# Kernel tuning notes

Measured on AMD Instinct MI355X. Metric: run time of the kernel, lower is better.

## Reference

```python
import jax, jax.numpy as jnp
import numpy as np

N = 50000   # nodes
E = 600000  # edges (time_feat is per-edge: same mask indexes k and src_idx)
D = 128     # adapter_dim
C = 8       # num_clusters
SCALE = D ** -0.5


def setup_inputs() -> dict:
    key = jax.random.key(0)
    ks = jax.random.split(key, 12)
    s = 1.0 / np.sqrt(D)
    return {
        "node_feat": jax.random.normal(ks[0], (N, D), jnp.float32),
        "time_feat": jax.random.normal(ks[1], (E, D), jnp.float32),
        "context_feat": jax.random.normal(ks[2], (N, D), jnp.float32),
        "edge_index": jax.random.randint(ks[3], (2, E), 0, N),
        "Wq": jax.random.uniform(ks[4], (D, D), jnp.float32, -s, s),
        "bq": jnp.zeros((D,), jnp.float32),
        "Wk": jax.random.uniform(ks[5], (D, D), jnp.float32, -s, s),
        "bk": jnp.zeros((D,), jnp.float32),
        "Wv": jax.random.uniform(ks[6], (D, D), jnp.float32, -s, s),
        "bv": jnp.zeros((D,), jnp.float32),
        "cluster_emb": jax.random.normal(ks[7], (C, D), jnp.float32),
        "Wo": jax.random.uniform(ks[8], (D, D), jnp.float32, -s, s),
        "bo": jnp.zeros((D,), jnp.float32),
    }


def reference(node_feat, time_feat, context_feat, edge_index,
              Wq, bq, Wk, bk, Wv, bv, cluster_emb, Wo, bo):
    q = node_feat @ Wq + bq            # [N, D]
    k = time_feat @ Wk + bk            # [E, D]
    v = time_feat @ Wv + bv            # [E, D]

    # cluster routing: argmax(softmax(sim)) == argmax(sim)
    sim = (time_feat @ cluster_emb.T) * SCALE   # [E, C]
    assign = jnp.argmax(sim, axis=-1)           # [E] int

    src = edge_index[0]                          # [E]
    seg = assign * N + src                       # combined (cluster, dst-of-scatter) segment id
    nseg = C * N

    attn = jnp.sum(q[src] * k, axis=-1) * SCALE  # [E]

    # scatter_softmax per (cluster, src node)
    seg_max = jax.ops.segment_max(attn, seg, num_segments=nseg)
    ex = jnp.exp(attn - seg_max[seg])
    denom = jax.ops.segment_sum(ex, seg, num_segments=nseg)
    w = ex / denom[seg]                          # [E]

    # scatter_mean per (cluster, src node) -> [C, N, D]
    wv = v * w[:, None]
    sums = jax.ops.segment_sum(wv, seg, num_segments=nseg)                 # [C*N, D]
    counts = jax.ops.segment_sum(jnp.ones((E,), v.dtype), seg, num_segments=nseg)
    means = sums / jnp.maximum(counts, 1.0)[:, None]                       # empty -> 0
    per_cluster = means.reshape(C, N, D)

    # sum(outputs) / len(outputs): only non-empty clusters contribute an entry
    edges_per_cluster = jax.ops.segment_sum(jnp.ones((E,), jnp.float32), assign, num_segments=C)
    num_nonempty = jnp.sum((edges_per_cluster > 0).astype(jnp.float32))
    combined = per_cluster.sum(axis=0) / num_nonempty                      # [N, D]

    return jax.nn.relu(combined @ Wo + bo)
```

## Files before the change

kernel.cpp:

```cpp
#include <hip/hip_runtime.h>
#include <math.h>


#define NN 50000
#define NE 600000
#define DD 128
#define NC 8
#define WIN 64
#define NWIN 9376
#define NBF  9377
#define CHK 32
#define NLOC 64
#define SCALEF 0.08838834764831845f

#define OFF_NODECNT  0
#define OFF_FILL     50000
#define OFF_MASK     100000
#define ZERO_ELEMS   100256
#define OFF_NODEOFF  100352
#define OFF_PARTIAL  150352
#define OFF_BF       150608
#define OFF_BQK      160000
#define OFF_BVO      160128
#define OFF_WQBK     160256
#define OFF_C0       160384
#define OFF_WQK      160400
#define OFF_WVO      176784
#define OFF_QB       193168
#define OFF_SORTED   243168
#define OFF_SRCS     843168
#define OFF_SW       1443168
#define OFF_P        1493168

__global__ __launch_bounds__(256) void k_pre_count(
    const float* __restrict__ Wq, const float* __restrict__ bq,
    const float* __restrict__ Wk, const float* __restrict__ bk,
    const float* __restrict__ Wv, const float* __restrict__ bv,
    const float* __restrict__ Wo, const int* __restrict__ ei,
    int* __restrict__ node_cnt,
    float* __restrict__ Wqk, float* __restrict__ bqk,
    float* __restrict__ Wvo, float* __restrict__ bvo,
    float* __restrict__ wqbk, float* __restrict__ c0) {
  int bid = blockIdx.x, t = threadIdx.x;
  if (bid >= 129) {
    long e = (long)(bid - 129) * 256 + t;
    if (e < NE) atomicAdd(&node_cnt[ei[e]], 1);
    return;
  }
  __shared__ float rq[DD], rv[DD];
  int b = bid;
  if (b < DD) {
    if (t < DD) { rq[t] = Wq[b * DD + t]; rv[t] = Wv[b * DD + t]; }
    __syncthreads();
    if (t < DD) {
      float aq = 0.f, av = 0.f;
      for (int j = 0; j < DD; j++) {
        aq += rq[j] * Wk[t * DD + j];
        av += rv[j] * Wo[j * DD + t];
      }
      Wqk[b * DD + t] = aq;
      Wvo[b * DD + t] = av;
    }
  } else {
    if (t < DD) {
      float a1 = 0.f, a2 = 0.f, a3 = 0.f;
      for (int j = 0; j < DD; j++) {
        a1 += bq[j] * Wk[t * DD + j];
        a2 += bv[j] * Wo[j * DD + t];
        a3 += Wq[t * DD + j] * bk[j];
      }
      bqk[t] = a1; bvo[t] = a2; wqbk[t] = a3;
      if (t == 0) {
        float s = 0.f;
        for (int j = 0; j < DD; j++) s += bq[j] * bk[j];
        *c0 = s;
      }
    }
  }
}

__global__ __launch_bounds__(256) void k_p(
    const float* __restrict__ nf, const float* __restrict__ Wqk,
    const float* __restrict__ bqk, const float* __restrict__ wqbk,
    const float* __restrict__ c0p,
    float* __restrict__ p, float* __restrict__ qb) {
  __shared__ float a_lds[64 * DD];
  __shared__ float wb_lds[DD];
  int t = threadIdx.x;
  long row0 = (long)blockIdx.x * 64;
  for (int it = 0; it < 8; it++) {
    int idx = (it * 256 + t) * 4;
    long r = row0 + idx / DD;
    float4 v = {0.f, 0.f, 0.f, 0.f};
    if (r < NN) v = *(const float4*)(nf + r * DD + (idx % DD));
    *(float4*)(a_lds + idx) = v;
  }
  if (t < DD) wb_lds[t] = wqbk[t];
  __syncthreads();
  int cg = t % 32, rg = t / 32;
  int col0 = cg * 4, r0 = rg * 8;
  float acc[8][4]; float qacc[8];
  for (int r = 0; r < 8; r++) { qacc[r] = 0.f; for (int c = 0; c < 4; c++) acc[r][c] = 0.f; }
  for (int k = 0; k < DD; k++) {
    float4 b4 = *(const float4*)(Wqk + k * DD + col0);
    float wbk = wb_lds[k];
    for (int r = 0; r < 8; r++) {
      float a = a_lds[(r0 + r) * DD + k];
      acc[r][0] += a * b4.x; acc[r][1] += a * b4.y;
      acc[r][2] += a * b4.z; acc[r][3] += a * b4.w;
      qacc[r] += a * wbk;
    }
  }
  float4 bq4 = *(const float4*)(bqk + col0);
  float c0v = *c0p;
  for (int r = 0; r < 8; r++) {
    long row = row0 + r0 + r;
    if (row < NN) {
      float4 o;
      o.x = acc[r][0] + bq4.x; o.y = acc[r][1] + bq4.y;
      o.z = acc[r][2] + bq4.z; o.w = acc[r][3] + bq4.w;
      *(float4*)(p + row * DD + col0) = o;
      if (cg == 0) qb[row] = qacc[r] + c0v;
    }
  }
}

__global__ __launch_bounds__(256) void k_scan1(const int* __restrict__ node_cnt,
                                               int* __restrict__ partial) {
  int i = blockIdx.x * 256 + threadIdx.x;
  int v = (i < NN) ? node_cnt[i] : 0;
  for (int o = 1; o < 64; o <<= 1) v += __shfl_xor(v, o);
  __shared__ int wsum[4];
  if ((threadIdx.x & 63) == 0) wsum[threadIdx.x >> 6] = v;
  __syncthreads();
  if (threadIdx.x == 0) partial[blockIdx.x] = wsum[0] + wsum[1] + wsum[2] + wsum[3];
}

__global__ __launch_bounds__(256) void k_scan2(int* __restrict__ partial) {
  __shared__ int s[256];
  int t = threadIdx.x;
  int v = (t < 196) ? partial[t] : 0;
  s[t] = v;
  __syncthreads();
  for (int o = 1; o < 256; o <<= 1) {
    int add = (t >= o) ? s[t - o] : 0;
    __syncthreads();
    s[t] += add;
    __syncthreads();
  }
  if (t < 196) partial[t] = s[t] - v;
}

__global__ __launch_bounds__(256) void k_scan3(const int* __restrict__ node_cnt,
                                               const int* __restrict__ partial,
                                               int* __restrict__ node_off) {
  __shared__ int s[256];
  int t = threadIdx.x;
  int i = blockIdx.x * 256 + t;
  int v = (i < NN) ? node_cnt[i] : 0;
  s[t] = v;
  __syncthreads();
  for (int o = 1; o < 256; o <<= 1) {
    int add = (t >= o) ? s[t - o] : 0;
    __syncthreads();
    s[t] += add;
    __syncthreads();
  }
  if (i < NN) node_off[i] = partial[blockIdx.x] + s[t] - v;
}

#define EDGE_BLKS 2344
#define BS_BLKS   37
__global__ __launch_bounds__(256) void k_scatter(const int* __restrict__ ei,
                                                 const int* __restrict__ node_off,
                                                 int* __restrict__ fill,
                                                 int* __restrict__ sorted,
                                                 int* __restrict__ srcs,
                                                 int* __restrict__ blockFirst) {
  int bid = blockIdx.x, t = threadIdx.x;
  if (bid >= EDGE_BLKS) {
    int w = (bid - EDGE_BLKS) * 256 + t;
    if (w < NBF) {
      int v = w * WIN, lo = 0, hi = NN;
      while (lo < hi) { int mid = (lo + hi) >> 1; if (node_off[mid] < v) lo = mid + 1; else hi = mid; }
      blockFirst[w] = lo;
    }
    return;
  }
  long e = (long)bid * 256 + t;
  if (e < NE) {
    int s = ei[e];
    int pos = node_off[s] + atomicAdd(&fill[s], 1);
    sorted[pos] = (int)e;
    srcs[pos] = s;
  }
}

__global__ __launch_bounds__(256) void k_fused2(
    const float* __restrict__ tf, const int* __restrict__ sorted,
    const int* __restrict__ srcs, const int* __restrict__ node_off,
    const int* __restrict__ node_cnt, const int* __restrict__ blockFirst,
    const float* __restrict__ ce, const float* __restrict__ p,
    const float* __restrict__ qb, int* __restrict__ maskArr,
    float* __restrict__ agg, float* __restrict__ sw) {
  __shared__ float ce_lds[NC * DD];
  __shared__ float t_lds[CHK * DD];
  __shared__ float U_sh[NC * DD];
  __shared__ float D_sh[NLOC * NC];
  __shared__ int   C_sh[NLOC * NC];
  __shared__ float exf_sh[CHK];
  __shared__ int   cli_sh[CHK];
  __shared__ int   eidx_sh[CHK];
  __shared__ int   srcs_sh[CHK];
  __shared__ int   cnt0_sh[NLOC];

  int t = threadIdx.x, b = blockIdx.x;
  int fn = blockFirst[b], ln = blockFirst[b + 1] - 1;
  if (fn >= NN || ln < fn) return;

  *(float4*)(ce_lds + t * 4) = *(const float4*)(ce + t * 4);

  int el = t >> 3, j = t & 7;
  int d = t & 127;
  int msk_acc = 0;

  for (int s0 = fn; s0 <= ln; s0 += NLOC) {
    int e2 = s0 + NLOC - 1; if (e2 > ln) e2 = ln;
    int nN = e2 - s0 + 1;
    int eb = node_off[s0];
    int ee = node_off[e2] + node_cnt[e2];
    for (int i = t; i < NLOC * NC; i += 256) { D_sh[i] = 0.f; C_sh[i] = 0; }
    for (int i = t; i < NC * DD; i += 256) U_sh[i] = 0.f;
    if (t < nN) cnt0_sh[t] = node_cnt[s0 + t];
    __syncthreads();

    for (int n = 0; n < nN; n++) {
      if (cnt0_sh[n] == 0) {
        if (t < DD) agg[(long)(s0 + n) * DD + t] = 0.f;
        if (t == 0) sw[s0 + n] = 0.f;
      }
    }

    int cur = -1;
    auto do_flush = [&](int node) {
      int l = (node - s0) * NC;
      if (t < DD) {
        float acc = 0.f;
        #pragma unroll
        for (int c = 0; c < NC; c++) {
          int cc = C_sh[l + c];
          if (cc > 0)
            acc += U_sh[c * DD + d] * __builtin_amdgcn_rcpf(D_sh[l + c] * (float)cc);
          U_sh[c * DD + d] = 0.f;
        }
        agg[(long)node * DD + d] = acc;
      }
      if (t == 0) {
        float ssw = 0.f; int mk = 0;
        #pragma unroll
        for (int c = 0; c < NC; c++) {
          int cc = C_sh[l + c];
          if (cc > 0) { mk |= 1 << c; ssw += __builtin_amdgcn_rcpf((float)cc); }
        }
        sw[node] = ssw; msk_acc |= mk;
      }
    };

    for (int c0 = eb; c0 < ee; c0 += CHK) {
      int m = ee - c0; if (m > CHK) m = CHK;
      if (t < m) { eidx_sh[t] = sorted[c0 + t]; srcs_sh[t] = srcs[c0 + t]; }
      __syncthreads();

      if (el < m) {
        long eid = eidx_sh[el];
        int src = srcs_sh[el];
        const float* trow = tf + eid * DD;
        const float* prow = p + (long)src * DD;
        float4 tv[4];
        #pragma unroll
        for (int i = 0; i < 4; i++) tv[i] = *(const float4*)(trow + (i * 8 + j) * 4);
        int sw8 = el & 7;
        #pragma unroll
        for (int i = 0; i < 4; i++)
          *(float4*)(t_lds + el * DD + (((i * 8 + j) ^ sw8) << 2)) = tv[i];
        float a = 0.f;
        #pragma unroll
        for (int i = 0; i < 4; i++) {
          float4 pv = *(const float4*)(prow + (i * 8 + j) * 4);
          a += tv[i].x * pv.x + tv[i].y * pv.y + tv[i].z * pv.z + tv[i].w * pv.w;
        }
        float sims[NC];
        #pragma unroll
        for (int c = 0; c < NC; c++) {
          const float* cr = ce_lds + c * DD;
          float sacc = 0.f;
          #pragma unroll
          for (int i = 0; i < 4; i++) {
            float4 cv = *(const float4*)(cr + (i * 8 + j) * 4);
            sacc += tv[i].x * cv.x + tv[i].y * cv.y + tv[i].z * cv.z + tv[i].w * cv.w;
          }
          sims[c] = sacc;
        }
        #pragma unroll
        for (int c = 0; c < NC; c++) {
          sims[c] += __shfl_xor(sims[c], 1);
          sims[c] += __shfl_xor(sims[c], 2);
          sims[c] += __shfl_xor(sims[c], 4);
        }
        a += __shfl_xor(a, 1);
        a += __shfl_xor(a, 2);
        a += __shfl_xor(a, 4);
        if (j == 0) {
          float best = sims[0]; int bc = 0;
          #pragma unroll
          for (int c = 1; c < NC; c++) if (sims[c] > best) { best = sims[c]; bc = c; }
          float ex = expf((a + qb[src]) * SCALEF);
          exf_sh[el] = ex; cli_sh[el] = bc;
          int l = (src - s0) * NC + bc;
          atomicAdd(&D_sh[l], ex);
          atomicAdd(&C_sh[l], 1);
        }
      }
      __syncthreads();

      for (int ii = 0; ii < m; ii++) {
        int sv = srcs_sh[ii];
        if (sv != cur) {
          if (cur >= 0) do_flush(cur);
          cur = sv;
        }
        if (t < DD) {
          int c = cli_sh[ii];
          float tval = t_lds[ii * DD + ((((d >> 2) ^ (ii & 7)) << 2) | (d & 3))];
          U_sh[c * DD + d] += exf_sh[ii] * tval;
        }
      }
      __syncthreads();
    }
    if (cur >= 0) do_flush(cur);
    __syncthreads();
  }
  if (t == 0 && msk_acc) atomicOr(&maskArr[b & 255], msk_acc);
}

__global__ __launch_bounds__(256) void k_out(
    const float* __restrict__ agg, const float* __restrict__ Wvo,
    const float* __restrict__ bvo, const float* __restrict__ sw,
    const float* __restrict__ bo, const int* __restrict__ maskArr,
    float* __restrict__ out) {
  __shared__ float a_lds[64 * DD];
  __shared__ float sw_lds[64];
  __shared__ int morw[4];
  int t = threadIdx.x;
  int mv = maskArr[t];
  for (int o = 1; o < 64; o <<= 1) mv |= __shfl_xor(mv, o);
  if ((t & 63) == 0) morw[t >> 6] = mv;
  long row0 = (long)blockIdx.x * 64;
  for (int it = 0; it < 8; it++) {
    int idx = (it * 256 + t) * 4;
    long r = row0 + idx / DD;
    float4 v = {0.f, 0.f, 0.f, 0.f};
    if (r < NN) v = *(const float4*)(agg + r * DD + (idx % DD));
    *(float4*)(a_lds + idx) = v;
  }
  if (t < 64) {
    long r = row0 + t;
    sw_lds[t] = (r < NN) ? sw[r] : 0.f;
  }
  __syncthreads();
  int full = morw[0] | morw[1] | morw[2] | morw[3];
  int nne = __popc(full); if (nne == 0) nne = 1;
  float inv = 1.0f / (float)nne;
  int cg = t % 32, rg = t / 32;
  int col0 = cg * 4, r0 = rg * 8;
  float acc[8][4];
  for (int r = 0; r < 8; r++) for (int c = 0; c < 4; c++) acc[r][c] = 0.f;
  for (int k = 0; k < DD; k++) {
    float4 b4 = *(const float4*)(Wvo + k * DD + col0);
    for (int r = 0; r < 8; r++) {
      float a = a_lds[(r0 + r) * DD + k];
      acc[r][0] += a * b4.x; acc[r][1] += a * b4.y;
      acc[r][2] += a * b4.z; acc[r][3] += a * b4.w;
    }
  }
  float4 bv4 = *(const float4*)(bvo + col0);
  float4 bo4 = *(const float4*)(bo + col0);
  for (int r = 0; r < 8; r++) {
    long row = row0 + r0 + r;
    if (row < NN) {
      float s = sw_lds[r0 + r];
      float4 o;
      o.x = fmaxf((acc[r][0] + s * bv4.x) * inv + bo4.x, 0.f);
      o.y = fmaxf((acc[r][1] + s * bv4.y) * inv + bo4.y, 0.f);
      o.z = fmaxf((acc[r][2] + s * bv4.z) * inv + bo4.z, 0.f);
      o.w = fmaxf((acc[r][3] + s * bv4.w) * inv + bo4.w, 0.f);
      *(float4*)(out + row * DD + col0) = o;
    }
  }
}

extern "C" void kernel_launch(void* const* d_in, const int* in_sizes, int n_in,
                              void* d_out, int out_size, void* d_ws, size_t ws_size,
                              hipStream_t stream) {
  const float* nf = (const float*)d_in[0];
  const float* tf = (const float*)d_in[1];
  const int*   ei = (const int*)d_in[3];
  const float* Wq = (const float*)d_in[4];
  const float* bq = (const float*)d_in[5];
  const float* Wk = (const float*)d_in[6];
  const float* bk = (const float*)d_in[7];
  const float* Wv = (const float*)d_in[8];
  const float* bv = (const float*)d_in[9];
  const float* ce = (const float*)d_in[10];
  const float* Wo = (const float*)d_in[11];
  const float* bo = (const float*)d_in[12];
  float* out = (float*)d_out;

  float* ws  = (float*)d_ws;
  int*   node_cnt = (int*)(ws + OFF_NODECNT);
  int*   fill     = (int*)(ws + OFF_FILL);
  int*   maskArr  = (int*)(ws + OFF_MASK);
  int*   node_off = (int*)(ws + OFF_NODEOFF);
  int*   partial  = (int*)(ws + OFF_PARTIAL);
  int*   blockFirst = (int*)(ws + OFF_BF);
  float* bqk      = ws + OFF_BQK;
  float* bvo      = ws + OFF_BVO;
  float* wqbk     = ws + OFF_WQBK;
  float* c0       = ws + OFF_C0;
  float* Wqk      = ws + OFF_WQK;
  float* Wvo      = ws + OFF_WVO;
  float* qb       = ws + OFF_QB;
  int*   sorted   = (int*)(ws + OFF_SORTED);
  int*   srcs     = (int*)(ws + OFF_SRCS);
  float* sw       = ws + OFF_SW;
  float* p        = ws + OFF_P;
  float* agg      = ws + OFF_P;

  hipMemsetAsync(d_ws, 0, (size_t)ZERO_ELEMS * 4, stream);

  k_pre_count<<<129 + EDGE_BLKS, 256, 0, stream>>>(
      Wq, bq, Wk, bk, Wv, bv, Wo, ei, node_cnt, Wqk, bqk, Wvo, bvo, wqbk, c0);
  k_p<<<(NN + 63) / 64, 256, 0, stream>>>(nf, Wqk, bqk, wqbk, c0, p, qb);
  k_scan1<<<196, 256, 0, stream>>>(node_cnt, partial);
  k_scan2<<<1, 256, 0, stream>>>(partial);
  k_scan3<<<196, 256, 0, stream>>>(node_cnt, partial, node_off);
  k_scatter<<<EDGE_BLKS + BS_BLKS, 256, 0, stream>>>(ei, node_off, fill, sorted,
                                                     srcs, blockFirst);
  k_fused2<<<NWIN, 256, 0, stream>>>(tf, sorted, srcs, node_off, node_cnt,
                                     blockFirst, ce, p, qb, maskArr, agg, sw);
  k_out<<<(NN + 63) / 64, 256, 0, stream>>>(agg, Wvo, bvo, sw, bo, maskArr, out);
}
```

Before: 745.1 us.

## Restructure fused edge kernel to stage whole node groups and parallelize aggregation

```diff
diff --git a/kernel.cpp b/kernel.cpp
--- a/kernel.cpp
+++ b/kernel.cpp
@@ -9,8 +9,8 @@
 #define WIN 64
 #define NWIN 9376
 #define NBF  9377
-#define CHK 32
-#define NLOC 64
+#define EC 84
+#define NLOC 32
 #define SCALEF 0.08838834764831845f
 
 #define OFF_NODECNT  0
@@ -196,23 +196,80 @@
   }
 }
 
-__global__ __launch_bounds__(256) void k_fused2(
+__device__ __forceinline__ void phase_a(
+    const float* __restrict__ tf, const float* __restrict__ p,
+    const float* __restrict__ qb,
+    const float* ce_lds, float* t_lds, float* exf_sh, int* cli_sh,
+    float* D_sh, int* C_sh,
+    int el, int j, int eid, int src, int lnode, bool doStage, bool doDC) {
+  const float* trow = tf + (long)eid * DD;
+  float4 tv[8];
+  #pragma unroll
+  for (int i = 0; i < 8; i++) tv[i] = *(const float4*)(trow + (j * 8 + i) * 4);
+  if (doStage) {
+    int e7 = el & 7;
+    #pragma unroll
+    for (int i = 0; i < 8; i++)
+      *(float4*)(t_lds + el * DD + (((j * 8 + i) ^ e7) << 2)) = tv[i];
+  }
+  const float* prow = p + (long)src * DD;
+  float a = 0.f;
+  #pragma unroll
+  for (int i = 0; i < 8; i++) {
+    float4 pv = *(const float4*)(prow + (j * 8 + i) * 4);
+    a += tv[i].x * pv.x + tv[i].y * pv.y + tv[i].z * pv.z + tv[i].w * pv.w;
+  }
+  float sims[NC];
+  #pragma unroll
+  for (int c = 0; c < NC; c++) {
+    const float* cr = ce_lds + c * DD;
+    float s = 0.f;
+    #pragma unroll
+    for (int i = 0; i < 8; i++) {
+      float4 cv = *(const float4*)(cr + (j * 8 + i) * 4);
+      s += tv[i].x * cv.x + tv[i].y * cv.y + tv[i].z * cv.z + tv[i].w * cv.w;
+    }
+    sims[c] = s;
+  }
+  #pragma unroll
+  for (int c = 0; c < NC; c++) {
+    sims[c] += __shfl_xor(sims[c], 1);
+    sims[c] += __shfl_xor(sims[c], 2);
+  }
+  a += __shfl_xor(a, 1);
+  a += __shfl_xor(a, 2);
+  if (j == 0) {
+    float best = sims[0]; int bc = 0;
+    #pragma unroll
+    for (int c = 1; c < NC; c++) if (sims[c] > best) { best = sims[c]; bc = c; }
+    float ex = expf((a + qb[src]) * SCALEF);
+    exf_sh[el] = ex; cli_sh[el] = bc;
+    if (doDC) {
+      atomicAdd(&D_sh[lnode * NC + bc], ex);
+      atomicAdd(&C_sh[lnode * NC + bc], 1);
+    }
+  }
+}
+
+__global__ __launch_bounds__(256) void k_fused3(
     const float* __restrict__ tf, const int* __restrict__ sorted,
     const int* __restrict__ srcs, const int* __restrict__ node_off,
     const int* __restrict__ node_cnt, const int* __restrict__ blockFirst,
     const float* __restrict__ ce, const float* __restrict__ p,
     const float* __restrict__ qb, int* __restrict__ maskArr,
     float* __restrict__ agg, float* __restrict__ sw) {
+  __shared__ float t_lds[EC * DD];
   __shared__ float ce_lds[NC * DD];
-  __shared__ float t_lds[CHK * DD];
-  __shared__ float U_sh[NC * DD];
+  __shared__ float exf_sh[EC];
+  __shared__ float scl_sh[EC];
+  __shared__ int   cli_sh[EC];
+  __shared__ int   eidx_sh[EC];
+  __shared__ int   srcs_sh[EC];
+  __shared__ int   offL_sh[NLOC];
+  __shared__ int   cntL_sh[NLOC];
   __shared__ float D_sh[NLOC * NC];
   __shared__ int   C_sh[NLOC * NC];
-  __shared__ float exf_sh[CHK];
-  __shared__ int   cli_sh[CHK];
-  __shared__ int   eidx_sh[CHK];
-  __shared__ int   srcs_sh[CHK];
-  __shared__ int   cnt0_sh[NLOC];
+  __shared__ int   ctrl[4];
 
   int t = threadIdx.x, b = blockIdx.x;
   int fn = blockFirst[b], ln = blockFirst[b + 1] - 1;
@@ -220,127 +277,130 @@
 
   *(float4*)(ce_lds + t * 4) = *(const float4*)(ce + t * 4);
 
-  int el = t >> 3, j = t & 7;
-  int d = t & 127;
-  int msk_acc = 0;
-
-  for (int s0 = fn; s0 <= ln; s0 += NLOC) {
-    int e2 = s0 + NLOC - 1; if (e2 > ln) e2 = ln;
-    int nN = e2 - s0 + 1;
-    int eb = node_off[s0];
-    int ee = node_off[e2] + node_cnt[e2];
+  int el4 = t >> 2, j4 = t & 3;
+  int team = t >> 6, d2 = (t & 63) * 2;
+  int msk = 0;
+
+  int s0 = fn;
+  while (s0 <= ln) {
+    if (t < 64) {
+      int offv = 0, cntv = 0; bool fit = false;
+      if (t < NLOC && s0 + t <= ln) { offv = node_off[s0 + t]; cntv = node_cnt[s0 + t]; }
+      int off0 = __shfl(offv, 0);
+      if (t < NLOC && s0 + t <= ln) fit = (offv - off0 + cntv) <= EC;
+      unsigned long long bm = __ballot(fit);
+      int pref = (int)__popcll(bm);
+      if (t < pref) { offL_sh[t] = offv - off0; cntL_sh[t] = cntv; }
+      if (t == 0) { ctrl[0] = pref; ctrl[2] = off0; ctrl[3] = cntv; }
+      if (pref > 0 && t == pref - 1) ctrl[1] = offv - off0 + cntv;
+    }
     for (int i = t; i < NLOC * NC; i += 256) { D_sh[i] = 0.f; C_sh[i] = 0; }
-    for (int i = t; i < NC * DD; i += 256) U_sh[i] = 0.f;
-    if (t < nN) cnt0_sh[t] = node_cnt[s0 + t];
-    __syncthreads();
-
-    for (int n = 0; n < nN; n++) {
-      if (cnt0_sh[n] == 0) {
-        if (t < DD) agg[(long)(s0 + n) * DD + t] = 0.f;
-        if (t == 0) sw[s0 + n] = 0.f;
-      }
-    }
-
-    int cur = -1;
-    auto do_flush = [&](int node) {
-      int l = (node - s0) * NC;
-      if (t < DD) {
-        float acc = 0.f;
+    __syncthreads();
+    int nN = ctrl[0], eb = ctrl[2];
+
+    if (nN == 0) {
+      int cnt = ctrl[3];
+      for (int c0 = 0; c0 < cnt; c0 += 64) {
+        int m = cnt - c0; if (m > 64) m = 64;
+        if (t < m) eidx_sh[t] = sorted[eb + c0 + t];
+        __syncthreads();
+        if (el4 < m)
+          phase_a(tf, p, qb, ce_lds, t_lds, exf_sh, cli_sh, D_sh, C_sh,
+                  el4, j4, eidx_sh[el4], s0, 0, false, true);
+        __syncthreads();
+      }
+      float r0a = 0.f, r1a = 0.f;
+      for (int c0 = 0; c0 < cnt; c0 += EC) {
+        int m = cnt - c0; if (m > EC) m = EC;
+        if (t < m) eidx_sh[t] = sorted[eb + c0 + t];
+        __syncthreads();
+        for (int r0 = 0; r0 < m; r0 += 64) {
+          int el = r0 + el4;
+          if (el < m)
+            phase_a(tf, p, qb, ce_lds, t_lds, exf_sh, cli_sh, D_sh, C_sh,
+                    el, j4, eidx_sh[el], s0, 0, true, false);
+        }
+        __syncthreads();
+        if (t < m) {
+          int c = cli_sh[t];
+          scl_sh[t] = exf_sh[t] * __builtin_amdgcn_rcpf(D_sh[c] * (float)C_sh[c]);
+        }
+        __syncthreads();
+        for (int e = team; e < m; e += 4) {
+          float s = scl_sh[e];
+          const float* tp = t_lds + e * DD + ((((d2 >> 2) ^ (e & 7)) << 2) | (d2 & 3));
+          r0a += s * tp[0]; r1a += s * tp[1];
+        }
+        __syncthreads();
+      }
+      *(float2*)(t_lds + team * DD + d2) = make_float2(r0a, r1a);
+      __syncthreads();
+      if (team == 0) {
+        float s0v = 0.f, s1v = 0.f;
         #pragma unroll
-        for (int c = 0; c < NC; c++) {
-          int cc = C_sh[l + c];
-          if (cc > 0)
-            acc += U_sh[c * DD + d] * __builtin_amdgcn_rcpf(D_sh[l + c] * (float)cc);
-          U_sh[c * DD + d] = 0.f;
+        for (int tm = 0; tm < 4; tm++) {
+          s0v += t_lds[tm * DD + d2]; s1v += t_lds[tm * DD + d2 + 1];
         }
-        agg[(long)node * DD + d] = acc;
+        *(float2*)(agg + (long)s0 * DD + d2) = make_float2(s0v, s1v);
       }
       if (t == 0) {
         float ssw = 0.f; int mk = 0;
         #pragma unroll
         for (int c = 0; c < NC; c++) {
-          int cc = C_sh[l + c];
+          int cc = C_sh[c];
           if (cc > 0) { mk |= 1 << c; ssw += __builtin_amdgcn_rcpf((float)cc); }
         }
-        sw[node] = ssw; msk_acc |= mk;
-      }
-    };
-
-    for (int c0 = eb; c0 < ee; c0 += CHK) {
-      int m = ee - c0; if (m > CHK) m = CHK;
-      if (t < m) { eidx_sh[t] = sorted[c0 + t]; srcs_sh[t] = srcs[c0 + t]; }
+        sw[s0] = ssw; msk |= mk;
+      }
       __syncthreads();
-
-      if (el < m) {
-        long eid = eidx_sh[el];
+      s0 += 1;
+      continue;
+    }
+
+    int span = ctrl[1];
+    if (t < span) { eidx_sh[t] = sorted[eb + t]; srcs_sh[t] = srcs[eb + t]; }
+    __syncthreads();
+
+    for (int r0 = 0; r0 < span; r0 += 64) {
+      int el = r0 + el4;
+      if (el < span) {
         int src = srcs_sh[el];
-        const float* trow = tf + eid * DD;
-        const float* prow = p + (long)src * DD;
-        float4 tv[4];
-        #pragma unroll
-        for (int i = 0; i < 4; i++) tv[i] = *(const float4*)(trow + (i * 8 + j) * 4);
-        int sw8 = el & 7;
-        #pragma unroll
-        for (int i = 0; i < 4; i++)
-          *(float4*)(t_lds + el * DD + (((i * 8 + j) ^ sw8) << 2)) = tv[i];
-        float a = 0.f;
-        #pragma unroll
-        for (int i = 0; i < 4; i++) {
-          float4 pv = *(const float4*)(prow + (i * 8 + j) * 4);
-          a += tv[i].x * pv.x + tv[i].y * pv.y + tv[i].z * pv.z + tv[i].w * pv.w;
-        }
-        float sims[NC];
+        phase_a(tf, p, qb, ce_lds, t_lds, exf_sh, cli_sh, D_sh, C_sh,
+                el, j4, eidx_sh[el], src, src - s0, true, true);
+      }
+    }
+    __syncthreads();
+
+    if (t < span) {
+      int l = (srcs_sh[t] - s0) * NC + cli_sh[t];
+      scl_sh[t] = exf_sh[t] * __builtin_amdgcn_rcpf(D_sh[l] * (float)C_sh[l]);
+    }
+    __syncthreads();
+
+    for (int k = team; k < nN; k += 4) {
+      float r0a = 0.f, r1a = 0.f;
+      int e1 = offL_sh[k] + cntL_sh[k];
+      for (int e = offL_sh[k]; e < e1; e++) {
+        float s = scl_sh[e];
+        const float* tp = t_lds + e * DD + ((((d2 >> 2) ^ (e & 7)) << 2) | (d2 & 3));
+        r0a += s * tp[0]; r1a += s * tp[1];
+      }
+      long n = s0 + k;
+      *(float2*)(agg + n * DD + d2) = make_float2(r0a, r1a);
+      if ((t & 63) == 0) {
+        float ssw = 0.f; int mk = 0;
         #pragma unroll
         for (int c = 0; c < NC; c++) {
-          const float* cr = ce_lds + c * DD;
-          float sacc = 0.f;
-          #pragma unroll
-          for (int i = 0; i < 4; i++) {
-            float4 cv = *(const float4*)(cr + (i * 8 + j) * 4);
-            sacc += tv[i].x * cv.x + tv[i].y * cv.y + tv[i].z * cv.z + tv[i].w * cv.w;
-          }
-          sims[c] = sacc;
+          int cc = C_sh[k * NC + c];
+          if (cc > 0) { mk |= 1 << c; ssw += __builtin_amdgcn_rcpf((float)cc); }
         }
-        #pragma unroll
-        for (int c = 0; c < NC; c++) {
-          sims[c] += __shfl_xor(sims[c], 1);
-          sims[c] += __shfl_xor(sims[c], 2);
-          sims[c] += __shfl_xor(sims[c], 4);
-        }
-        a += __shfl_xor(a, 1);
-        a += __shfl_xor(a, 2);
-        a += __shfl_xor(a, 4);
-        if (j == 0) {
-          float best = sims[0]; int bc = 0;
-          #pragma unroll
-          for (int c = 1; c < NC; c++) if (sims[c] > best) { best = sims[c]; bc = c; }
-          float ex = expf((a + qb[src]) * SCALEF);
-          exf_sh[el] = ex; cli_sh[el] = bc;
-          int l = (src - s0) * NC + bc;
-          atomicAdd(&D_sh[l], ex);
-          atomicAdd(&C_sh[l], 1);
-        }
-      }
-      __syncthreads();
-
-      for (int ii = 0; ii < m; ii++) {
-        int sv = srcs_sh[ii];
-        if (sv != cur) {
-          if (cur >= 0) do_flush(cur);
-          cur = sv;
-        }
-        if (t < DD) {
-          int c = cli_sh[ii];
-          float tval = t_lds[ii * DD + ((((d >> 2) ^ (ii & 7)) << 2) | (d & 3))];
-          U_sh[c * DD + d] += exf_sh[ii] * tval;
-        }
-      }
-      __syncthreads();
-    }
-    if (cur >= 0) do_flush(cur);
-    __syncthreads();
-  }
-  if (t == 0 && msk_acc) atomicOr(&maskArr[b & 255], msk_acc);
+        sw[n] = ssw; msk |= mk;
+      }
+    }
+    __syncthreads();
+    s0 += nN;
+  }
+  if (msk) atomicOr(&maskArr[b & 255], msk);
 }
 
 __global__ __launch_bounds__(256) void k_out(
@@ -446,7 +506,7 @@
   k_scan3<<<196, 256, 0, stream>>>(node_cnt, partial, node_off);
   k_scatter<<<EDGE_BLKS + BS_BLKS, 256, 0, stream>>>(ei, node_off, fill, sorted,
                                                      srcs, blockFirst);
-  k_fused2<<<NWIN, 256, 0, stream>>>(tf, sorted, srcs, node_off, node_cnt,
+  k_fused3<<<NWIN, 256, 0, stream>>>(tf, sorted, srcs, node_off, node_cnt,
                                      blockFirst, ce, p, qb, maskArr, agg, sw);
   k_out<<<(NN + 63) / 64, 256, 0, stream>>>(agg, Wvo, bvo, sw, bo, maskArr, out);
 }
```

After: 688.5 us. 1.08x faster.
